# Kernel tuning notes

Measured on AMD Instinct MI355X. Metric: run time of the kernel, lower is better.

Reference implementation:

```python
import jax, jax.numpy as jnp
import numpy as np

OT_REG = 0.1      # entropic regularization (ot_reg)
OT_TAU = 0.5      # marginal relaxation (ot_tau / reg_m)
N_ITERS = 100     # fixed Sinkhorn iterations (POT uses numItermax=1000 w/ stopThr=1e-6; 100 is converged here)


def setup_inputs() -> dict:
    key = jax.random.key(0)
    k1, k2 = jax.random.split(key)
    x = jax.random.normal(k1, (1, 4096, 1024), dtype=jnp.float32)
    y = jax.random.normal(k2, (1, 2048, 1024), dtype=jnp.float32)
    return {"x": x, "y": y}


def _sq_cdist(a, b):
    # torch.cdist(a, b) ** 2  ==  squared Euclidean pairwise distances, [N, M]
    d = (jnp.sum(a * a, axis=1)[:, None]
         + jnp.sum(b * b, axis=1)[None, :]
         - 2.0 * (a @ b.T))
    return jnp.maximum(d, 0.0)


def reference(x, y):
    # forward: squeeze leading batch dim, shift features to be >= 0 per row
    x = jnp.squeeze(x, axis=0)                      # [N, D]
    y = jnp.squeeze(y, axis=0)                      # [M, D]
    x = x - jnp.min(x, axis=-1, keepdims=True)
    y = y - jnp.min(y, axis=-1, keepdims=True)

    C = _sq_cdist(x, y)                              # [N, M] cost map (differentiable)
    n, m = C.shape

    # POT sinkhorn_knopp_unbalanced on detached, max-normalized cost
    Mn = jax.lax.stop_gradient(C)
    Mn = Mn / jnp.max(Mn)
    K = jnp.exp(-Mn / OT_REG)                        # Gibbs kernel
    a = jnp.full((n,), 1.0 / n, dtype=C.dtype)       # uniform source marginal
    b = jnp.full((m,), 1.0 / m, dtype=C.dtype)       # uniform target marginal
    fi = OT_TAU / (OT_TAU + OT_REG)

    def body(i, uv):
        u, v = uv
        u = (a / (K @ v)) ** fi
        v = (b / (K.T @ u)) ** fi
        return (u, v)

    u0 = jnp.full((n,), 1.0 / n, dtype=C.dtype)
    v0 = jnp.full((m,), 1.0 / m, dtype=C.dtype)
    u, v = jax.lax.fori_loop(0, N_ITERS, body, (u0, v0))

    flow = u[:, None] * K * v[None, :]               # [N, M] transport plan
    flow = jax.lax.stop_gradient(flow)               # plan is detached in original (numpy roundtrip)
    dist = jnp.sum(C * flow)                         # OT distance w/ grad through C only

    return flow.T[None], dist                        # pi.T.unsqueeze(0): [1, M, N]
```

## Files before the change

### kernel.cpp

```cpp
#include <hip/hip_runtime.h>


#define NROWS 4096
#define MCOLS 2048
#define NITER 100
#define NBLK  256
#define SPEC_TICKS 85ull

using short8  = __attribute__((ext_vector_type(8))) short;
using floatx4 = __attribute__((ext_vector_type(4))) float;

__device__ __forceinline__ float bf2f(unsigned short u) {
  return __uint_as_float(((unsigned)u) << 16);
}
__device__ __forceinline__ unsigned short f2bf(float f) {
  unsigned u = __float_as_uint(f);
  u += 0x7fffu + ((u >> 16) & 1u);
  return (unsigned short)(u >> 16);
}
__device__ __forceinline__ float powfi(float x, float fi) {
  return __expf(fi * __logf(x));
}
__device__ __forceinline__ unsigned packsp(float v, unsigned parity) {
  return __float_as_uint(v) | (parity << 31);
}
__device__ __forceinline__ unsigned aload(const unsigned* p) {
  return __hip_atomic_load(p, __ATOMIC_RELAXED, __HIP_MEMORY_SCOPE_AGENT);
}
__device__ __forceinline__ void astore(unsigned* p, unsigned v) {
  __hip_atomic_store(p, v, __ATOMIC_RELAXED, __HIP_MEMORY_SCOPE_AGENT);
}

__global__ __launch_bounds__(256) void prep_kernel(
    const float* __restrict__ x, const float* __restrict__ y,
    unsigned short* __restrict__ xb, unsigned short* __restrict__ yb,
    float* __restrict__ nx, float* __restrict__ ny,
    unsigned* __restrict__ maxCbits, float* __restrict__ out,
    unsigned* __restrict__ uglob, unsigned* __restrict__ vglob,
    unsigned* __restrict__ ublkflag, unsigned* __restrict__ vblkflag,
    unsigned* __restrict__ uroot, unsigned* __restrict__ vroot) {
  const int row = blockIdx.x;
  const int tid = threadIdx.x;

  if (row == 0) {
    if (tid == 0) { *maxCbits = 0u; out[8388608] = 0.0f; }
    #pragma unroll
    for (int k = 0; k < 16; ++k) uglob[tid + (k << 8)] = 0u;
    #pragma unroll
    for (int k = 0; k < 8; ++k) vglob[tid + (k << 8)] = 0u;
    ublkflag[tid] = 0u;
    vblkflag[tid] = 0u;
    if (tid < 32) { uroot[tid * 32] = 0u; vroot[tid * 32] = 0u; }
  }

  const float* src; unsigned short* dst; float* nd;
  if (row < NROWS) { src = x + (size_t)row * 1024; dst = xb + (size_t)row * 1024; nd = nx + row; }
  else { const int r = row - NROWS; src = y + (size_t)r * 1024; dst = yb + (size_t)r * 1024; nd = ny + r; }

  float4 v = ((const float4*)src)[tid];
  float mn = fminf(fminf(v.x, v.y), fminf(v.z, v.w));
  #pragma unroll
  for (int m = 1; m < 64; m <<= 1) mn = fminf(mn, __shfl_xor(mn, m));
  __shared__ float wred[4];
  const int w = tid >> 6, l = tid & 63;
  if (l == 0) wred[w] = mn;
  __syncthreads();
  mn = fminf(fminf(wred[0], wred[1]), fminf(wred[2], wred[3]));
  __syncthreads();

  const unsigned short b0 = f2bf(v.x - mn), b1 = f2bf(v.y - mn);
  const unsigned short b2 = f2bf(v.z - mn), b3 = f2bf(v.w - mn);
  ushort4 ub; ub.x = b0; ub.y = b1; ub.z = b2; ub.w = b3;
  ((ushort4*)dst)[tid] = ub;
  const float f0 = bf2f(b0), f1 = bf2f(b1), f2 = bf2f(b2), f3 = bf2f(b3);
  float acc = f0 * f0 + f1 * f1 + f2 * f2 + f3 * f3;
  #pragma unroll
  for (int m = 1; m < 64; m <<= 1) acc += __shfl_xor(acc, m);
  if (l == 0) wred[w] = acc;
  __syncthreads();
  if (tid == 0) *nd = wred[0] + wred[1] + wred[2] + wred[3];
}

__global__ __launch_bounds__(256) void cost_gemm_kernel(
    const unsigned short* __restrict__ xb, const unsigned short* __restrict__ yb,
    const float* __restrict__ nx, const float* __restrict__ ny,
    float* __restrict__ C, unsigned* __restrict__ maxCbits) {
  const int tid = threadIdx.x;
  const int w = tid >> 6, l = tid & 63;
  const int wr = w >> 1, wc = w & 1;
  const int i0 = blockIdx.y * 128 + wr * 64;
  const int j0 = blockIdx.x * 128 + wc * 64;
  const int m16 = l & 15, q = l >> 4;

  const unsigned short* ap = xb + (size_t)(i0 + m16) * 1024 + q * 8;
  const unsigned short* bp = yb + (size_t)(j0 + m16) * 1024 + q * 8;

  floatx4 acc[4][4];
  #pragma unroll
  for (int a = 0; a < 4; ++a)
    #pragma unroll
    for (int b = 0; b < 4; ++b) acc[a][b] = (floatx4){0.f, 0.f, 0.f, 0.f};

  for (int k0 = 0; k0 < 1024; k0 += 32) {
    short8 av[4], bv[4];
    #pragma unroll
    for (int t = 0; t < 4; ++t) av[t] = *(const short8*)(ap + (size_t)t * 16 * 1024 + k0);
    #pragma unroll
    for (int t = 0; t < 4; ++t) bv[t] = *(const short8*)(bp + (size_t)t * 16 * 1024 + k0);
    #pragma unroll
    for (int ti = 0; ti < 4; ++ti)
      #pragma unroll
      for (int tj = 0; tj < 4; ++tj)
        acc[ti][tj] = __builtin_amdgcn_mfma_f32_16x16x32_bf16(av[ti], bv[tj], acc[ti][tj], 0, 0, 0);
  }

  float mx = 0.f;
  #pragma unroll
  for (int ti = 0; ti < 4; ++ti) {
    #pragma unroll
    for (int tj = 0; tj < 4; ++tj) {
      const int i = i0 + ti * 16 + q * 4;
      const int j = j0 + tj * 16 + m16;
      const float nyj = ny[j];
      #pragma unroll
      for (int r = 0; r < 4; ++r) {
        float c = nx[i + r] + nyj - 2.0f * acc[ti][tj][r];
        c = fmaxf(c, 0.0f);
        C[(size_t)(i + r) * 2048 + j] = c;
        mx = fmaxf(mx, c);
      }
    }
  }
  __shared__ float mred[4];
  #pragma unroll
  for (int m = 1; m < 64; m <<= 1) mx = fmaxf(mx, __shfl_xor(mx, m));
  if (l == 0) mred[w] = mx;
  __syncthreads();
  if (tid == 0) {
    const float bm = fmaxf(fmaxf(mred[0], mred[1]), fmaxf(mred[2], mred[3]));
    atomicMax(maxCbits, __float_as_uint(bm));
  }
}

__global__ __launch_bounds__(512) void sinkhorn_kernel(
    const float* __restrict__ C, const unsigned* __restrict__ maxCbits,
    unsigned* __restrict__ uglob, unsigned* __restrict__ vglob,
    unsigned* __restrict__ ublkflag, unsigned* __restrict__ vblkflag,
    unsigned* __restrict__ uroot, unsigned* __restrict__ vroot,
    float* __restrict__ out) {
  __shared__ __align__(16) unsigned short Ks[16 * 2048];
  __shared__ __align__(16) unsigned short KsT[8 * 4096];
  __shared__ __align__(16) float us[4096];
  __shared__ __align__(16) float vs[2048];
  __shared__ __align__(16) float uloc[16];
  __shared__ float dred[8];
  __shared__ unsigned needretry;

  const int tid = threadIdx.x;
  const int bid = blockIdx.x;
  const int w = tid >> 6, l = tid & 63;
  const int i0 = bid * 16;
  const int jb = bid * 8;

  const float fi = 0.8333333333333334f;
  const float av = 1.0f / 4096.0f;
  const float bv = 1.0f / 2048.0f;

  {
    if (tid == 0) needretry = 0u;
    const float sc = -1.0f / (0.1f * __uint_as_float(*maxCbits));
    for (int il = 0; il < 16; ++il) {
      const float* cp = C + (size_t)(i0 + il) * 2048 + tid * 4;
      const float4 c0 = *(const float4*)cp;
      uint2 pk;
      pk.x = (unsigned)f2bf(__expf(c0.x * sc)) | ((unsigned)f2bf(__expf(c0.y * sc)) << 16);
      pk.y = (unsigned)f2bf(__expf(c0.z * sc)) | ((unsigned)f2bf(__expf(c0.w * sc)) << 16);
      *(uint2*)&Ks[il * 2048 + tid * 4] = pk;
    }
    #pragma unroll
    for (int k = 0; k < 8; ++k) {
      const int i = tid + (k << 9);
      const float* cp = C + (size_t)i * 2048 + jb;
      const float4 c0 = *(const float4*)cp;
      const float4 c1 = *(const float4*)(cp + 4);
      KsT[0 * 4096 + i] = f2bf(__expf(c0.x * sc));
      KsT[1 * 4096 + i] = f2bf(__expf(c0.y * sc));
      KsT[2 * 4096 + i] = f2bf(__expf(c0.z * sc));
      KsT[3 * 4096 + i] = f2bf(__expf(c0.w * sc));
      KsT[4 * 4096 + i] = f2bf(__expf(c1.x * sc));
      KsT[5 * 4096 + i] = f2bf(__expf(c1.y * sc));
      KsT[6 * 4096 + i] = f2bf(__expf(c1.z * sc));
      KsT[7 * 4096 + i] = f2bf(__expf(c1.w * sc));
    }
    *(float4*)&vs[tid * 4] = make_float4(bv, bv, bv, bv);
  }
  __syncthreads();

  for (int it = 1; it <= NITER; ++it) {
    const unsigned tagit = (unsigned)it;
    const unsigned par = tagit & 1u;

    float part[2] = {0.f, 0.f};
    const int r0 = w * 2;
    #pragma unroll
    for (int c = 0; c < 4; ++c) {
      const int j0 = c * 512 + l * 8;
      const float4 va = *(const float4*)&vs[j0];
      const float4 vb = *(const float4*)&vs[j0 + 4];
      #pragma unroll
      for (int rr = 0; rr < 2; ++rr) {
        const uint4 kb = *(const uint4*)&Ks[(r0 + rr) * 2048 + j0];
        part[rr] += bf2f((unsigned short)kb.x) * va.x + bf2f((unsigned short)(kb.x >> 16)) * va.y
                 +  bf2f((unsigned short)kb.y) * va.z + bf2f((unsigned short)(kb.y >> 16)) * va.w
                 +  bf2f((unsigned short)kb.z) * vb.x + bf2f((unsigned short)(kb.z >> 16)) * vb.y
                 +  bf2f((unsigned short)kb.w) * vb.z + bf2f((unsigned short)(kb.w >> 16)) * vb.w;
      }
    }
    #pragma unroll
    for (int m = 1; m < 64; m <<= 1) {
      part[0] += __shfl_xor(part[0], m);
      part[1] += __shfl_xor(part[1], m);
    }
    if (l == 0) {
      #pragma unroll
      for (int r = 0; r < 2; ++r) {
        const float uv = powfi(av / part[r], fi);
        uloc[r0 + r] = uv;
        astore(&uglob[i0 + r0 + r], packsp(uv, par));
      }
    }
    __builtin_amdgcn_s_barrier();
    if (tid == 0) astore(&ublkflag[bid], tagit);
    const unsigned long long udl = __builtin_amdgcn_s_memrealtime() + SPEC_TICKS;

    if (bid == 0) {
      if (tid < 256)
        while ((int)(aload(&ublkflag[tid]) - tagit) < 0) __builtin_amdgcn_s_sleep(1);
      __builtin_amdgcn_s_barrier();
      if (tid < 32) astore(&uroot[tid * 32], tagit);
    }

    while (__builtin_amdgcn_s_memrealtime() < udl) __builtin_amdgcn_s_sleep(1);
    {
      unsigned pend = 0xFFu;
      unsigned gu[8];
      #pragma unroll
      for (int k = 0; k < 8; ++k)
        gu[k] = aload(&uglob[tid + (k << 9)]);
      #pragma unroll
      for (int k = 0; k < 8; ++k)
        if ((gu[k] >> 31) == par) {
          us[tid + (k << 9)] = __uint_as_float(gu[k] & 0x7FFFFFFFu);
          pend &= ~(1u << k);
        }
      if (pend) {
        #pragma unroll
        for (int k = 0; k < 8; ++k)
          if (pend & (1u << k))
            gu[k] = aload(&uglob[tid + (k << 9)]);
        #pragma unroll
        for (int k = 0; k < 8; ++k)
          if ((pend & (1u << k)) && (gu[k] >> 31) == par) {
            us[tid + (k << 9)] = __uint_as_float(gu[k] & 0x7FFFFFFFu);
            pend &= ~(1u << k);
          }
      }
      if (pend) atomicOr(&needretry, 1u);
      __syncthreads();
      if (needretry) {
        if (tid == 0)
          while ((int)(aload(&uroot[(bid & 31) * 32]) - tagit) < 0) __builtin_amdgcn_s_sleep(1);
        __syncthreads();
        while (pend) {
          #pragma unroll
          for (int k = 0; k < 8; ++k)
            if (pend & (1u << k))
              gu[k] = aload(&uglob[tid + (k << 9)]);
          #pragma unroll
          for (int k = 0; k < 8; ++k)
            if ((pend & (1u << k)) && (gu[k] >> 31) == par) {
              us[tid + (k << 9)] = __uint_as_float(gu[k] & 0x7FFFFFFFu);
              pend &= ~(1u << k);
            }
          if (pend) __builtin_amdgcn_s_sleep(1);
        }
        if (tid == 0) needretry = 0u;
        __syncthreads();
      }
    }

    {
      float t0 = 0.f;
      const int ca = w * 4096;
      #pragma unroll
      for (int c = 0; c < 8; ++c) {
        const int ic = c * 512 + l * 8;
        const float4 ua = *(const float4*)&us[ic];
        const float4 ub = *(const float4*)&us[ic + 4];
        const uint4 ka = *(const uint4*)&KsT[ca + ic];
        t0 += bf2f((unsigned short)ka.x) * ua.x + bf2f((unsigned short)(ka.x >> 16)) * ua.y
           +  bf2f((unsigned short)ka.y) * ua.z + bf2f((unsigned short)(ka.y >> 16)) * ua.w
           +  bf2f((unsigned short)ka.z) * ub.x + bf2f((unsigned short)(ka.z >> 16)) * ub.y
           +  bf2f((unsigned short)ka.w) * ub.z + bf2f((unsigned short)(ka.w >> 16)) * ub.w;
      }
      #pragma unroll
      for (int m = 1; m < 64; m <<= 1) t0 += __shfl_xor(t0, m);
      if (l == 0)
        astore(&vglob[jb + w], packsp(powfi(bv / t0, fi), par));
    }
    __builtin_amdgcn_s_barrier();
    if (tid == 0) astore(&vblkflag[bid], tagit);
    const unsigned long long vdl = __builtin_amdgcn_s_memrealtime() + SPEC_TICKS;

    if (bid == 1) {
      if (tid < 256)
        while ((int)(aload(&vblkflag[tid]) - tagit) < 0) __builtin_amdgcn_s_sleep(1);
      __builtin_amdgcn_s_barrier();
      if (tid < 32) astore(&vroot[tid * 32], tagit);
    }

    while (__builtin_amdgcn_s_memrealtime() < vdl) __builtin_amdgcn_s_sleep(1);
    {
      unsigned pend = 0xFu;
      unsigned gv[4];
      #pragma unroll
      for (int k = 0; k < 4; ++k)
        gv[k] = aload(&vglob[tid + (k << 9)]);
      #pragma unroll
      for (int k = 0; k < 4; ++k)
        if ((gv[k] >> 31) == par) {
          vs[tid + (k << 9)] = __uint_as_float(gv[k] & 0x7FFFFFFFu);
          pend &= ~(1u << k);
        }
      if (pend) {
        #pragma unroll
        for (int k = 0; k < 4; ++k)
          if (pend & (1u << k))
            gv[k] = aload(&vglob[tid + (k << 9)]);
        #pragma unroll
        for (int k = 0; k < 4; ++k)
          if ((pend & (1u << k)) && (gv[k] >> 31) == par) {
            vs[tid + (k << 9)] = __uint_as_float(gv[k] & 0x7FFFFFFFu);
            pend &= ~(1u << k);
          }
      }
      if (pend) atomicOr(&needretry, 1u);
      __syncthreads();
      if (needretry) {
        if (tid == 0)
          while ((int)(aload(&vroot[(bid & 31) * 32]) - tagit) < 0) __builtin_amdgcn_s_sleep(1);
        __syncthreads();
        while (pend) {
          #pragma unroll
          for (int k = 0; k < 4; ++k)
            if (pend & (1u << k))
              gv[k] = aload(&vglob[tid + (k << 9)]);
          #pragma unroll
          for (int k = 0; k < 4; ++k)
            if ((pend & (1u << k)) && (gv[k] >> 31) == par) {
              vs[tid + (k << 9)] = __uint_as_float(gv[k] & 0x7FFFFFFFu);
              pend &= ~(1u << k);
            }
          if (pend) __builtin_amdgcn_s_sleep(1);
        }
        if (tid == 0) needretry = 0u;
        __syncthreads();
      }
    }
  }

  float ur[16];
  *(float4*)&ur[0]  = *(const float4*)&uloc[0];
  *(float4*)&ur[4]  = *(const float4*)&uloc[4];
  *(float4*)&ur[8]  = *(const float4*)&uloc[8];
  *(float4*)&ur[12] = *(const float4*)&uloc[12];
  float distp = 0.f;
  for (int sub = 0; sub < 4; ++sub) {
    const int j = w * 256 + sub * 64 + l;
    const float vj = vs[j];
    float o[16];
    #pragma unroll
    for (int il = 0; il < 16; ++il) {
      const float kf = bf2f(Ks[il * 2048 + j]);
      const float fl = ur[il] * kf * vj;
      o[il] = fl;
      distp += C[(size_t)(i0 + il) * 2048 + j] * fl;
    }
    float* op = out + (size_t)j * 4096 + i0;
    *(float4*)(op)      = make_float4(o[0],  o[1],  o[2],  o[3]);
    *(float4*)(op + 4)  = make_float4(o[4],  o[5],  o[6],  o[7]);
    *(float4*)(op + 8)  = make_float4(o[8],  o[9],  o[10], o[11]);
    *(float4*)(op + 12) = make_float4(o[12], o[13], o[14], o[15]);
  }
  #pragma unroll
  for (int m = 1; m < 64; m <<= 1) distp += __shfl_xor(distp, m);
  if (l == 0) dred[w] = distp;
  __syncthreads();
  if (tid == 0) {
    float ds = 0.f;
    #pragma unroll
    for (int k = 0; k < 8; ++k) ds += dred[k];
    unsafeAtomicAdd(out + (size_t)8388608, ds);
  }
}

extern "C" void kernel_launch(void* const* d_in, const int* in_sizes, int n_in,
                              void* d_out, int out_size, void* d_ws, size_t ws_size,
                              hipStream_t stream) {
  (void)in_sizes; (void)n_in; (void)out_size; (void)ws_size;
  const float* x = (const float*)d_in[0];
  const float* y = (const float*)d_in[1];
  float* out = (float*)d_out;
  char* ws = (char*)d_ws;

  float*              Cmat     = (float*)(ws + 0);
  unsigned short*     xb       = (unsigned short*)(ws + 33554432);
  unsigned short*     yb       = (unsigned short*)(ws + 41943040);
  float*              nx       = (float*)(ws + 46137344);
  float*              ny       = (float*)(ws + 46153728);
  unsigned*           maxC     = (unsigned*)(ws + 46161920);
  unsigned*           uglob    = (unsigned*)(ws + 46162432);
  unsigned*           vglob    = (unsigned*)(ws + 46178816);
  unsigned*           ublkflag = (unsigned*)(ws + 46187008);
  unsigned*           vblkflag = (unsigned*)(ws + 46188032);
  unsigned*           uroot    = (unsigned*)(ws + 46189056);
  unsigned*           vroot    = (unsigned*)(ws + 46193152);

  hipLaunchKernelGGL(prep_kernel, dim3(6144), dim3(256), 0, stream, x, y, xb, yb, nx, ny,
                     maxC, out, uglob, vglob, ublkflag, vblkflag, uroot, vroot);
  hipLaunchKernelGGL(cost_gemm_kernel, dim3(16, 32), dim3(256), 0, stream, xb, yb, nx, ny, Cmat, maxC);
  hipLaunchKernelGGL(sinkhorn_kernel, dim3(NBLK), dim3(512), 0, stream,
                     Cmat, maxC, uglob, vglob, ublkflag, vblkflag, uroot, vroot, out);
}
```

Measured before the change: 677.5 us.

## Stage cost GEMM tiles through LDS with direct global-to-LDS loads and swizzle

Moves the cost-matrix GEMM from per-wave direct global loads to block-shared LDS tiles, filled with global_load_lds (16 bytes per lane) and read back through an XOR swizzle that avoids bank conflicts. The 128x64 A and B tiles are shared by all four waves, so each input element is fetched from global memory once per block rather than by two waves. The K step doubles to 64 with two barriers per iteration and no double buffering, so load latency is not overlapped with MFMA work. The GEMM is only one part of a pipeline that is mostly Sinkhorn iterations, so the end-to-end effect is limited.

```diff
diff --git a/kernel.cpp b/kernel.cpp
--- a/kernel.cpp
+++ b/kernel.cpp
@@ -29,6 +29,11 @@
 }
 __device__ __forceinline__ void astore(unsigned* p, unsigned v) {
   __hip_atomic_store(p, v, __ATOMIC_RELAXED, __HIP_MEMORY_SCOPE_AGENT);
+}
+__device__ __forceinline__ void gload_lds16(const unsigned short* gsrc, unsigned short* ldst) {
+  __builtin_amdgcn_global_load_lds(
+      (const __attribute__((address_space(1))) void*)gsrc,
+      (__attribute__((address_space(3))) void*)ldst, 16, 0, 0);
 }
 
 __global__ __launch_bounds__(256) void prep_kernel(
@@ -85,15 +90,18 @@
     const unsigned short* __restrict__ xb, const unsigned short* __restrict__ yb,
     const float* __restrict__ nx, const float* __restrict__ ny,
     float* __restrict__ C, unsigned* __restrict__ maxCbits) {
+  __shared__ __align__(16) unsigned short As[128 * 64];
+  __shared__ __align__(16) unsigned short Bs[128 * 64];
+
   const int tid = threadIdx.x;
   const int w = tid >> 6, l = tid & 63;
   const int wr = w >> 1, wc = w & 1;
-  const int i0 = blockIdx.y * 128 + wr * 64;
-  const int j0 = blockIdx.x * 128 + wc * 64;
+  const int i0 = blockIdx.y * 128;
+  const int j0 = blockIdx.x * 128;
   const int m16 = l & 15, q = l >> 4;
 
-  const unsigned short* ap = xb + (size_t)(i0 + m16) * 1024 + q * 8;
-  const unsigned short* bp = yb + (size_t)(j0 + m16) * 1024 + q * 8;
+  const int st_row = tid >> 3;
+  const int st_s   = tid & 7;
 
   floatx4 acc[4][4];
   #pragma unroll
@@ -101,17 +109,45 @@
     #pragma unroll
     for (int b = 0; b < 4; ++b) acc[a][b] = (floatx4){0.f, 0.f, 0.f, 0.f};
 
-  for (int k0 = 0; k0 < 1024; k0 += 32) {
-    short8 av[4], bv[4];
-    #pragma unroll
-    for (int t = 0; t < 4; ++t) av[t] = *(const short8*)(ap + (size_t)t * 16 * 1024 + k0);
-    #pragma unroll
-    for (int t = 0; t < 4; ++t) bv[t] = *(const short8*)(bp + (size_t)t * 16 * 1024 + k0);
-    #pragma unroll
-    for (int ti = 0; ti < 4; ++ti)
-      #pragma unroll
-      for (int tj = 0; tj < 4; ++tj)
-        acc[ti][tj] = __builtin_amdgcn_mfma_f32_16x16x32_bf16(av[ti], bv[tj], acc[ti][tj], 0, 0, 0);
+  for (int k0 = 0; k0 < 1024; k0 += 64) {
+    #pragma unroll
+    for (int c = 0; c < 4; ++c) {
+      const int row = c * 32 + st_row;
+      const int ss = st_s ^ (row & 7);
+      gload_lds16(xb + (size_t)(i0 + row) * 1024 + k0 + ss * 8,
+                  &As[c * 2048 + tid * 8]);
+    }
+    #pragma unroll
+    for (int c = 0; c < 4; ++c) {
+      const int row = c * 32 + st_row;
+      const int ss = st_s ^ (row & 7);
+      gload_lds16(yb + (size_t)(j0 + row) * 1024 + k0 + ss * 8,
+                  &Bs[c * 2048 + tid * 8]);
+    }
+    __syncthreads();
+
+    #pragma unroll
+    for (int kk = 0; kk < 2; ++kk) {
+      short8 av[4], bv[4];
+      #pragma unroll
+      for (int t = 0; t < 4; ++t) {
+        const int row = wr * 64 + t * 16 + m16;
+        const int slot = (kk * 4 + q) ^ (row & 7);
+        av[t] = *(const short8*)&As[row * 64 + slot * 8];
+      }
+      #pragma unroll
+      for (int t = 0; t < 4; ++t) {
+        const int row = wc * 64 + t * 16 + m16;
+        const int slot = (kk * 4 + q) ^ (row & 7);
+        bv[t] = *(const short8*)&Bs[row * 64 + slot * 8];
+      }
+      #pragma unroll
+      for (int ti = 0; ti < 4; ++ti)
+        #pragma unroll
+        for (int tj = 0; tj < 4; ++tj)
+          acc[ti][tj] = __builtin_amdgcn_mfma_f32_16x16x32_bf16(av[ti], bv[tj], acc[ti][tj], 0, 0, 0);
+    }
+    __syncthreads();
   }
 
   float mx = 0.f;
@@ -119,8 +155,8 @@
   for (int ti = 0; ti < 4; ++ti) {
     #pragma unroll
     for (int tj = 0; tj < 4; ++tj) {
-      const int i = i0 + ti * 16 + q * 4;
-      const int j = j0 + tj * 16 + m16;
+      const int i = i0 + wr * 64 + ti * 16 + q * 4;
+      const int j = j0 + wc * 64 + tj * 16 + m16;
       const float nyj = ny[j];
       #pragma unroll
       for (int r = 0; r < 4; ++r) {
```

Result: faster. 638.5 us (-5.8%).
